# Performance work log

Hardware: AMD Instinct MI355X
Metric: run time of the kernel (lower is better)

Reference implementation:

```python
import jax, jax.numpy as jnp
import numpy as np

N_NODES = 50000
N_EDGES = 1600000
N_GRAPHS = 128
EDGE_DIM = 43
IN_DIM = 35
H = 128          # hidden_dim_1 = hidden_dim_2 = hidden_dim_3
G1, G2 = 64, 32  # gate MLP dims
H6, H7, H8 = 256, 128, 64
U0, U1 = 64, 64  # u_shape


def _linear_params(key, out_dim, in_dim):
    k1, k2 = jax.random.split(key)
    bound = 1.0 / np.sqrt(in_dim)
    W = jax.random.uniform(k1, (out_dim, in_dim), minval=-bound, maxval=bound, dtype=jnp.float32)
    b = jax.random.uniform(k2, (out_dim,), minval=-bound, maxval=bound, dtype=jnp.float32)
    return W, b


def setup_inputs() -> dict:
    key = jax.random.key(0)
    ks = jax.random.split(key, 24)
    x = jax.random.normal(ks[0], (N_NODES, IN_DIM), dtype=jnp.float32)
    edge_index = jax.random.randint(ks[1], (2, N_EDGES), 0, N_NODES, dtype=jnp.int64)
    edge_attr = jax.random.normal(ks[2], (N_EDGES, EDGE_DIM), dtype=jnp.float32)
    batch = jnp.sort(jax.random.randint(ks[3], (N_NODES,), 0, N_GRAPHS, dtype=jnp.int64))
    batch = batch.at[0].set(0).at[-1].set(N_GRAPHS - 1)
    u_soap = jax.random.normal(ks[4], (N_GRAPHS, U0), dtype=jnp.float32)
    u_dimer = jax.random.normal(ks[5], (N_GRAPHS, U1), dtype=jnp.float32)

    W1n, b1n = _linear_params(ks[6], H, IN_DIM + EDGE_DIM)
    W1r, b1r = _linear_params(ks[7], H, IN_DIM)
    W2n, b2n = _linear_params(ks[8], H, H + EDGE_DIM)
    W2r, b2r = _linear_params(ks[9], H, H)
    W3n, b3n = _linear_params(ks[10], H, H + EDGE_DIM)
    W3r, b3r = _linear_params(ks[11], H, H)
    Wg1, bg1 = _linear_params(ks[12], G1, H)
    Wg2, bg2 = _linear_params(ks[13], G2, G1)
    Wg3, bg3 = _linear_params(ks[14], 1, G2)
    Wl1, bl1 = _linear_params(ks[15], H6, U0 + U1 + H)
    Wl2, bl2 = _linear_params(ks[16], H7, H6)
    Wl3, bl3 = _linear_params(ks[17], H8, H7)
    Wl, bl = _linear_params(ks[18], 4, H8)

    return dict(x=x, edge_attr=edge_attr, u_soap=u_soap, u_dimer=u_dimer,
                W1n=W1n, b1n=b1n, W1r=W1r, b1r=b1r,
                W2n=W2n, b2n=b2n, W2r=W2r, b2r=b2r,
                W3n=W3n, b3n=b3n, W3r=W3r, b3r=b3r,
                Wg1=Wg1, bg1=bg1, Wg2=Wg2, bg2=bg2, Wg3=Wg3, bg3=bg3,
                Wl1=Wl1, bl1=bl1, Wl2=Wl2, bl2=bl2, Wl3=Wl3, bl3=bl3,
                Wl=Wl, bl=bl,
                edge_index=edge_index, batch=batch)


def _conv(x, src, edge_attr, Wn, bn, Wr, br):
    # gather source nodes, concat edge features, linear + tanh, scatter-add back to SOURCE (as in original)
    x_adj = jnp.tanh(jnp.concatenate([x[src], edge_attr], axis=1) @ Wn.T + bn)  # [E, H]
    neg_sum = jax.ops.segment_sum(x_adj, src, num_segments=N_NODES)             # [N, H]
    return jnp.tanh(x @ Wr.T + br) + neg_sum


def _segment_softmax(gate, batch, num_segments):
    m = jax.ops.segment_max(gate[:, 0], batch, num_segments=num_segments)
    g = jnp.exp(gate[:, 0] - m[batch])
    s = jax.ops.segment_sum(g, batch, num_segments=num_segments)
    return (g / (s[batch] + 1e-16))[:, None]


def reference(x, edge_attr, u_soap, u_dimer,
              W1n, b1n, W1r, b1r, W2n, b2n, W2r, b2r, W3n, b3n, W3r, b3r,
              Wg1, bg1, Wg2, bg2, Wg3, bg3,
              Wl1, bl1, Wl2, bl2, Wl3, bl3, Wl, bl,
              edge_index, batch):
    src = edge_index[0]
    h = _conv(x, src, edge_attr, W1n, b1n, W1r, b1r)
    h = _conv(h, src, edge_attr, W2n, b2n, W2r, b2r)
    h = _conv(h, src, edge_attr, W3n, b3n, W3r, b3r)

    # GlobalAttention readout
    g = jax.nn.relu(h @ Wg1.T + bg1)
    g = jax.nn.relu(g @ Wg2.T + bg2)
    gate = g @ Wg3.T + bg3                             # [N, 1]
    att = _segment_softmax(gate, batch, N_GRAPHS)      # [N, 1]
    embedding = jax.ops.segment_sum(att * h, batch, num_segments=N_GRAPHS)  # [G, H]

    u = jnp.concatenate([u_soap[:, :U0], u_dimer[:, :U1]], axis=1)
    e2 = jnp.concatenate([embedding, u], axis=1)
    out = jax.nn.relu(e2 @ Wl1.T + bl1)
    out = jax.nn.relu(out @ Wl2.T + bl2)
    out = jax.nn.relu(out @ Wl3.T + bl3)
    out4 = out @ Wl.T + bl                             # [G, 4]
    pred_last = out4.sum(axis=1, keepdims=True)
    return jnp.concatenate([out4, pred_last], axis=1), att
```

## Files before the change

kernel.cpp:

```cpp
#include <hip/hip_runtime.h>
#include <cstdint>
#include <cstddef>

#define N_NODES_C 50000
#define N_EDGES_C 1600000
#define N_GRAPHS_C 128
#define EDGE_DIM_C 43
#define IN_DIM_C 35
#define HDIM_C 128
#define MAXG_C 150000

typedef _Float16 f16x8 __attribute__((ext_vector_type(8)));
typedef float f32x4 __attribute__((ext_vector_type(4)));

__device__ __forceinline__ float fast_tanh(float x) {
    float xc = fminf(9.0f, fmaxf(-9.0f, x));
    float t = __expf(2.0f * xc);
    return (t - 1.0f) * __builtin_amdgcn_rcpf(t + 1.0f);
}


__global__ __launch_bounds__(256) void hist_kernel(const int* __restrict__ src,
                                                   int* __restrict__ cnt) {
    int i = blockIdx.x * 256 + threadIdx.x;
    if (i < N_EDGES_C) atomicAdd(&cnt[src[i]], 1);
}

__global__ __launch_bounds__(1024) void scan_kernel(const int* __restrict__ cnt,
                                                    int* __restrict__ rowptr,
                                                    int* __restrict__ work,
                                                    int* __restrict__ growptr,
                                                    int* __restrict__ ngroups) {
    __shared__ int wsumA[16], wsumB[16];
    __shared__ int carryA, carryB;
    int t = threadIdx.x;
    int lane = t & 63, wid = t >> 6;
    if (t == 0) { carryA = 0; carryB = 0; }
    __syncthreads();
    for (int base = 0; base < N_NODES_C; base += 4096) {
        int i0 = base + t * 4;
        int v[4], u[4];
        #pragma unroll
        for (int j = 0; j < 4; ++j) {
            int i = i0 + j;
            v[j] = (i < N_NODES_C) ? cnt[i] : 0;
            u[j] = (v[j] + 15) >> 4;
        }
        int pv[4], pu[4];
        pv[0] = 0; pu[0] = 0;
        #pragma unroll
        for (int j = 1; j < 4; ++j) { pv[j] = pv[j-1] + v[j-1]; pu[j] = pu[j-1] + u[j-1]; }
        int tA = pv[3] + v[3], tB = pu[3] + u[3];
        int x = tA, y = tB;
        #pragma unroll
        for (int off = 1; off < 64; off <<= 1) {
            int xx = __shfl_up(x, off, 64);
            int yy = __shfl_up(y, off, 64);
            if (lane >= off) { x += xx; y += yy; }
        }
        if (lane == 63) { wsumA[wid] = x; wsumB[wid] = y; }
        __syncthreads();
        if (wid == 0) {
            int wa = (lane < 16) ? wsumA[lane] : 0;
            int wb = (lane < 16) ? wsumB[lane] : 0;
            #pragma unroll
            for (int off = 1; off < 16; off <<= 1) {
                int aa = __shfl_up(wa, off, 64);
                int bb = __shfl_up(wb, off, 64);
                if (lane >= off) { wa += aa; wb += bb; }
            }
            if (lane < 16) { wsumA[lane] = wa; wsumB[lane] = wb; }
        }
        __syncthreads();
        int exA = carryA + (wid ? wsumA[wid - 1] : 0) + x - tA;
        int exB = carryB + (wid ? wsumB[wid - 1] : 0) + y - tB;
        #pragma unroll
        for (int j = 0; j < 4; ++j) {
            int i = i0 + j;
            if (i < N_NODES_C) {
                int rv = exA + pv[j];
                rowptr[i] = rv; work[i] = rv;
                growptr[i] = exB + pu[j];
            }
        }
        int totA = wsumA[15], totB = wsumB[15];
        __syncthreads();
        if (t == 0) { carryA += totA; carryB += totB; }
        __syncthreads();
    }
    if (t == 0) {
        rowptr[N_NODES_C] = carryA;
        growptr[N_NODES_C] = carryB;
        ngroups[0] = carryB;
    }
}

__global__ __launch_bounds__(256) void scatter_kernel(const int* __restrict__ src,
                                                      int* __restrict__ work,
                                                      int* __restrict__ epos) {
    int i = blockIdx.x * 256 + threadIdx.x;
    if (i < N_EDGES_C) {
        int s = src[i];
        int pos = atomicAdd(&work[s], 1);
        epos[i] = pos;
    }
}

__global__ __launch_bounds__(256) void graph_misc(const int* __restrict__ rowptr,
                                                  const int* __restrict__ growptr,
                                                  const int* __restrict__ batch,
                                                  int2* __restrict__ nmeta,
                                                  int* __restrict__ grp) {
    int i = blockIdx.x * 256 + threadIdx.x;
    if (i < N_NODES_C) {
        int deg = rowptr[i + 1] - rowptr[i];
        nmeta[i] = make_int2(deg, growptr[i]);
    }
    if (i <= N_GRAPHS_C) {
        int lo = 0, hi = N_NODES_C;
        while (lo < hi) {
            int mid = (lo + hi) >> 1;
            if (batch[mid] < i) lo = mid + 1; else hi = mid;
        }
        grp[i] = lo;
    }
}

__global__ __launch_bounds__(256) void pad_zero(const int2* __restrict__ nmeta,
                                                _Float16* __restrict__ EAp) {
    int id = blockIdx.x * 256 + threadIdx.x;
    int n = id >> 4, row = id & 15;
    if (n >= N_NODES_C) return;
    int2 nm = nmeta[n];
    int deg = nm.x;
    if (deg == 0) return;
    int rem = deg & 15;
    if (rem == 0 || row < rem) return;
    int g = nm.y + ((deg + 15) >> 4) - 1;
    uint2* dst = (uint2*)(EAp + (size_t)g * 768 + row * 48);
    uint2 z = make_uint2(0u, 0u);
    #pragma unroll
    for (int j = 0; j < 12; ++j) dst[j] = z;
}

__global__ __launch_bounds__(256) void permute_ea(const float* __restrict__ EA,
                                                  const int* __restrict__ src,
                                                  const int* __restrict__ epos,
                                                  const int* __restrict__ rowptr,
                                                  const int* __restrict__ growptr,
                                                  _Float16* __restrict__ EAp) {
    int t = threadIdx.x;
    int e = blockIdx.x * 64 + (t >> 2);
    int q = t & 3;
    if (e >= N_EDGES_C) return;
    int node = src[e];
    int pos = epos[e];
    int r = pos - rowptr[node];
    int g = growptr[node] + (r >> 4);
    int row = r & 15;

    const float* pe = EA + (size_t)e * EDGE_DIM_C;
    unsigned int pk[6];
    #pragma unroll
    for (int jj = 0; jj < 6; ++jj) {
        int c0 = q * 12 + 2 * jj;
        float v0 = (c0 < EDGE_DIM_C) ? pe[c0] : 0.0f;
        float v1 = (c0 + 1 < EDGE_DIM_C) ? pe[c0 + 1] : 0.0f;
        unsigned short h0 = __builtin_bit_cast(unsigned short, (_Float16)v0);
        unsigned short h1 = __builtin_bit_cast(unsigned short, (_Float16)v1);
        pk[jj] = (unsigned int)h0 | ((unsigned int)h1 << 16);
    }
    unsigned int* outp = (unsigned int*)(EAp + (size_t)g * 768 + row * 48 + q * 12);
    *(uint2*)(outp)     = make_uint2(pk[0], pk[1]);
    *(uint2*)(outp + 2) = make_uint2(pk[2], pk[3]);
    *(uint2*)(outp + 4) = make_uint2(pk[4], pk[5]);
}


#define BKN 32
__global__ __launch_bounds__(256) void node_gemm(
    const float* __restrict__ A, int K,
    const float* __restrict__ Wn, int ldn, const float* __restrict__ bn,
    const float* __restrict__ Wr, const float* __restrict__ br,
    float* __restrict__ Base, float* __restrict__ Root)
{
    __shared__ float At[BKN][64];
    __shared__ float Bw[BKN][128];
    int t = threadIdx.x;
    int z = blockIdx.y;
    const float* W = z ? Wr : Wn;
    int ldW = z ? K : ldn;
    const float* bias = z ? br : bn;
    float* Out = z ? Root : Base;

    int m0 = blockIdx.x * 64;
    int tn4 = (t % 32) * 4;
    int tm8 = (t / 32) * 8;
    float acc[8][4];
    #pragma unroll
    for (int a = 0; a < 8; a++)
        #pragma unroll
        for (int b = 0; b < 4; b++) acc[a][b] = 0.0f;

    int nkc = (K + BKN - 1) / BKN;
    for (int c = 0; c < nkc; c++) {
        int kc = c * BKN;
        {
            int m_l = t >> 2;
            int q = t & 3;
            int m = m0 + m_l;
            #pragma unroll
            for (int ii = 0; ii < 8; ii++) {
                int kk = q * 8 + ii;
                int k = kc + kk;
                float v = 0.0f;
                if (m < N_NODES_C && k < K) v = A[(size_t)m * K + k];
                At[kk][m_l] = v;
            }
        }
        {
            int j = t % 128;
            int kg2 = t / 128;
            #pragma unroll
            for (int ii = 0; ii < 16; ii++) {
                int kk = kg2 * 16 + ii;
                int k = kc + kk;
                float v = 0.0f;
                if (k < K) v = W[(size_t)j * ldW + k];
                Bw[kk][j] = v;
            }
        }
        __syncthreads();
        #pragma unroll
        for (int kk = 0; kk < BKN; kk++) {
            float a[8], b[4];
            #pragma unroll
            for (int mi = 0; mi < 8; mi++) a[mi] = At[kk][tm8 + mi];
            #pragma unroll
            for (int ni = 0; ni < 4; ni++) b[ni] = Bw[kk][tn4 + ni];
            #pragma unroll
            for (int mi = 0; mi < 8; mi++)
                #pragma unroll
                for (int ni = 0; ni < 4; ni++)
                    acc[mi][ni] = fmaf(a[mi], b[ni], acc[mi][ni]);
        }
        __syncthreads();
    }

    float4 bv = *(const float4*)&bias[tn4];
    #pragma unroll
    for (int mi = 0; mi < 8; mi++) {
        int m = m0 + tm8 + mi;
        if (m < N_NODES_C) {
            float4 o;
            o.x = acc[mi][0] + bv.x;
            o.y = acc[mi][1] + bv.y;
            o.z = acc[mi][2] + bv.z;
            o.w = acc[mi][3] + bv.w;
            if (z) { o.x = fast_tanh(o.x); o.y = fast_tanh(o.y); o.z = fast_tanh(o.z); o.w = fast_tanh(o.w); }
            *(float4*)&Out[(size_t)m * HDIM_C + tn4] = o;
        }
    }
}


__global__ __launch_bounds__(256) void edge_mfma(
    const _Float16* __restrict__ EAp, const int2* __restrict__ nmeta,
    const float* __restrict__ Base, const float* __restrict__ Root,
    const float* __restrict__ Wfull, int colOff, int ldW,
    float* __restrict__ Hout)
{
    int t = threadIdx.x;
    int lane = t & 63, wid = t >> 6;
    int l15 = lane & 15, quad = lane >> 4;

    f16x8 bf[8][2];
    #pragma unroll
    for (int nt = 0; nt < 8; ++nt) {
        const float* wr = Wfull + (size_t)(nt * 16 + l15) * ldW + colOff;
        #pragma unroll
        for (int kt = 0; kt < 2; ++kt) {
            f16x8 b;
            #pragma unroll
            for (int j = 0; j < 8; ++j) {
                int k = kt * 32 + quad * 8 + j;
                float v = (k < EDGE_DIM_C) ? wr[k] : 0.0f;
                b[j] = (_Float16)v;
            }
            bf[nt][kt] = b;
        }
    }

    int aoff0 = l15 * 48 + quad * 8;
    int aoff1 = l15 * 48 + 32 + ((quad & 1) * 8);
    bool useA1 = (quad < 2);

    int nstride = gridDim.x * 4;
    for (int n = blockIdx.x * 4 + wid; n < N_NODES_C; n += nstride) {
        int2 nm = nmeta[n];
        int deg = nm.x, gptr = nm.y;
        const float* bp = Base + (size_t)n * HDIM_C;
        float bv[8];
        #pragma unroll
        for (int nt = 0; nt < 8; ++nt) bv[nt] = bp[nt * 16 + l15];
        float cs[8];
        #pragma unroll
        for (int nt = 0; nt < 8; ++nt) cs[nt] = 0.0f;

        int ngr = (deg + 15) >> 4;
        int rbase = quad * 4;
        if (ngr > 0) {
            const _Float16* apb = EAp + (size_t)gptr * 768;
            f16x8 zz8 = {};
            f16x8 a0 = *(const f16x8*)(apb + aoff0);
            f16x8 a1 = useA1 ? *(const f16x8*)(apb + aoff1) : zz8;
            for (int gi = 0; gi < ngr; ++gi) {
                f16x8 n0 = a0, n1 = a1;
                if (gi + 1 < ngr) {
                    const _Float16* apn = apb + (size_t)(gi + 1) * 768;
                    n0 = *(const f16x8*)(apn + aoff0);
                    n1 = useA1 ? *(const f16x8*)(apn + aoff1) : zz8;
                }
                int valid = deg - gi * 16; if (valid > 16) valid = 16;
                f32x4 acc[8];
                #pragma unroll
                for (int nt = 0; nt < 8; ++nt) {
                    f32x4 zz = {0.f, 0.f, 0.f, 0.f};
                    acc[nt] = __builtin_amdgcn_mfma_f32_16x16x32_f16(a0, bf[nt][0], zz, 0, 0, 0);
                    acc[nt] = __builtin_amdgcn_mfma_f32_16x16x32_f16(a1, bf[nt][1], acc[nt], 0, 0, 0);
                }
                #pragma unroll
                for (int nt = 0; nt < 8; ++nt) {
                    #pragma unroll
                    for (int r = 0; r < 4; ++r) {
                        float v = fast_tanh(acc[nt][r] + bv[nt]);
                        cs[nt] += (rbase + r < valid) ? v : 0.0f;
                    }
                }
                a0 = n0; a1 = n1;
            }
        }
        #pragma unroll
        for (int nt = 0; nt < 8; ++nt) {
            cs[nt] += __shfl_xor(cs[nt], 16, 64);
            cs[nt] += __shfl_xor(cs[nt], 32, 64);
        }
        float v0, v1;
        if (quad == 0)      { v0 = cs[0]; v1 = cs[1]; }
        else if (quad == 1) { v0 = cs[2]; v1 = cs[3]; }
        else if (quad == 2) { v0 = cs[4]; v1 = cs[5]; }
        else                { v0 = cs[6]; v1 = cs[7]; }
        int c0 = quad * 32 + l15;
        size_t rowb = (size_t)n * HDIM_C;
        Hout[rowb + c0]      = Root[rowb + c0] + v0;
        Hout[rowb + c0 + 16] = Root[rowb + c0 + 16] + v1;
    }
}


__global__ __launch_bounds__(256) void gate_kernel(
    const float* __restrict__ h,
    const float* __restrict__ Wg1, const float* __restrict__ bg1,
    const float* __restrict__ Wg2, const float* __restrict__ bg2,
    const float* __restrict__ Wg3, const float* __restrict__ bg3,
    float* __restrict__ gate)
{
    __shared__ float Ht[128][65];
    __shared__ float G1[64][65];
    __shared__ float G2[32][65];
    int t = threadIdx.x;
    int m0 = blockIdx.x * 64;
    #pragma unroll
    for (int ii = 0; ii < 32; ++ii) {
        int flat = ii * 256 + t;
        int k = flat & 127, m = flat >> 7;
        float v = (m0 + m < N_NODES_C) ? h[(size_t)(m0 + m) * HDIM_C + k] : 0.0f;
        Ht[k][m] = v;
    }
    __syncthreads();
    int m = t & 63, slab = t >> 6;
    {
        float a[16];
        #pragma unroll
        for (int jj = 0; jj < 16; ++jj) a[jj] = bg1[slab * 16 + jj];
        for (int k = 0; k < 128; ++k) {
            float hv = Ht[k][m];
            #pragma unroll
            for (int jj = 0; jj < 16; ++jj)
                a[jj] = fmaf(Wg1[(size_t)(slab * 16 + jj) * 128 + k], hv, a[jj]);
        }
        #pragma unroll
        for (int jj = 0; jj < 16; ++jj) G1[slab * 16 + jj][m] = fmaxf(a[jj], 0.0f);
    }
    __syncthreads();
    {
        float b[8];
        #pragma unroll
        for (int jj = 0; jj < 8; ++jj) b[jj] = bg2[slab * 8 + jj];
        for (int k = 0; k < 64; ++k) {
            float gv = G1[k][m];
            #pragma unroll
            for (int jj = 0; jj < 8; ++jj)
                b[jj] = fmaf(Wg2[(size_t)(slab * 8 + jj) * 64 + k], gv, b[jj]);
        }
        #pragma unroll
        for (int jj = 0; jj < 8; ++jj) G2[slab * 8 + jj][m] = fmaxf(b[jj], 0.0f);
    }
    __syncthreads();
    if (t < 64 && m0 + t < N_NODES_C) {
        float s = bg3[0];
        #pragma unroll
        for (int k = 0; k < 32; ++k) s = fmaf(Wg3[k], G2[k][t], s);
        gate[m0 + t] = s;
    }
}


__global__ __launch_bounds__(256) void graph_attn(
    const float* __restrict__ gate, const int* __restrict__ grp,
    const float* __restrict__ h3, float* __restrict__ att_out,
    float* __restrict__ emb)
{
    int g = blockIdx.x;
    int t = threadIdx.x;
    int s = grp[g], e = grp[g + 1];
    __shared__ float red[256];
    __shared__ float attb[256];

    float m = -3.4e38f;
    for (int i = s + t; i < e; i += 256) m = fmaxf(m, gate[i]);
    red[t] = m;
    __syncthreads();
    #pragma unroll
    for (int off = 128; off >= 1; off >>= 1) {
        if (t < off) red[t] = fmaxf(red[t], red[t + off]);
        __syncthreads();
    }
    m = red[0];
    __syncthreads();

    float sum = 0.0f;
    for (int i = s + t; i < e; i += 256) sum += __expf(gate[i] - m);
    red[t] = sum;
    __syncthreads();
    #pragma unroll
    for (int off = 128; off >= 1; off >>= 1) {
        if (t < off) red[t] += red[t + off];
        __syncthreads();
    }
    float scale = 1.0f / (red[0] + 1e-16f);
    __syncthreads();

    int j = t & 127;
    int half = t >> 7;
    float acc = 0.0f;
    for (int base = s; base < e; base += 256) {
        int i = base + t;
        float a = 0.0f;
        if (i < e) {
            a = __expf(gate[i] - m) * scale;
            att_out[i] = a;
        }
        attb[t] = a;
        __syncthreads();
        int cnt = e - base; if (cnt > 256) cnt = 256;
        for (int r = half; r < cnt; r += 2)
            acc = fmaf(attb[r], h3[(size_t)(base + r) * HDIM_C + j], acc);
        __syncthreads();
    }
    red[t] = acc;
    __syncthreads();
    if (t < 128) emb[(size_t)g * 128 + t] = red[t] + red[t + 128];
}


__global__ __launch_bounds__(256) void final_mlp(
    const float* __restrict__ emb, const float* __restrict__ us, const float* __restrict__ ud,
    const float* __restrict__ Wl1, const float* __restrict__ bl1,
    const float* __restrict__ Wl2, const float* __restrict__ bl2,
    const float* __restrict__ Wl3, const float* __restrict__ bl3,
    const float* __restrict__ Wl, const float* __restrict__ bl,
    float* __restrict__ out5)
{
    int g = blockIdx.x;
    int t = threadIdx.x;
    __shared__ float e2[256], o1[256], o2[128], o3[64], o4[4];
    if (t < 128) e2[t] = emb[(size_t)g * 128 + t];
    else if (t < 192) e2[t] = us[(size_t)g * 64 + (t - 128)];
    else e2[t] = ud[(size_t)g * 64 + (t - 192)];
    __syncthreads();
    {
        float s = bl1[t];
        const float* wr = Wl1 + (size_t)t * 256;
        #pragma unroll 8
        for (int k = 0; k < 256; k++) s = fmaf(wr[k], e2[k], s);
        o1[t] = fmaxf(s, 0.0f);
    }
    __syncthreads();
    if (t < 128) {
        float s = bl2[t];
        const float* wr = Wl2 + (size_t)t * 256;
        #pragma unroll 8
        for (int k = 0; k < 256; k++) s = fmaf(wr[k], o1[k], s);
        o2[t] = fmaxf(s, 0.0f);
    }
    __syncthreads();
    if (t < 64) {
        float s = bl3[t];
        const float* wr = Wl3 + (size_t)t * 128;
        #pragma unroll 8
        for (int k = 0; k < 128; k++) s = fmaf(wr[k], o2[k], s);
        o3[t] = fmaxf(s, 0.0f);
    }
    __syncthreads();
    if (t < 4) {
        float s = bl[t];
        const float* wr = Wl + (size_t)t * 64;
        #pragma unroll 8
        for (int k = 0; k < 64; k++) s = fmaf(wr[k], o3[k], s);
        o4[t] = s;
    }
    __syncthreads();
    if (t < 5) {
        float v = (t < 4) ? o4[t] : (o4[0] + o4[1] + o4[2] + o4[3]);
        out5[(size_t)g * 5 + t] = v;
    }
}


extern "C" void kernel_launch(void* const* d_in, const int* in_sizes, int n_in,
                              void* d_out, int out_size, void* d_ws, size_t ws_size,
                              hipStream_t stream) {
    const float* x       = (const float*)d_in[0];
    const float* ea      = (const float*)d_in[1];
    const float* u_soap  = (const float*)d_in[2];
    const float* u_dimer = (const float*)d_in[3];
    const float* W1n = (const float*)d_in[4];   const float* b1n = (const float*)d_in[5];
    const float* W1r = (const float*)d_in[6];   const float* b1r = (const float*)d_in[7];
    const float* W2n = (const float*)d_in[8];   const float* b2n = (const float*)d_in[9];
    const float* W2r = (const float*)d_in[10];  const float* b2r = (const float*)d_in[11];
    const float* W3n = (const float*)d_in[12];  const float* b3n = (const float*)d_in[13];
    const float* W3r = (const float*)d_in[14];  const float* b3r = (const float*)d_in[15];
    const float* Wg1 = (const float*)d_in[16];  const float* bg1 = (const float*)d_in[17];
    const float* Wg2 = (const float*)d_in[18];  const float* bg2 = (const float*)d_in[19];
    const float* Wg3 = (const float*)d_in[20];  const float* bg3 = (const float*)d_in[21];
    const float* Wl1 = (const float*)d_in[22];  const float* bl1 = (const float*)d_in[23];
    const float* Wl2 = (const float*)d_in[24];  const float* bl2 = (const float*)d_in[25];
    const float* Wl3 = (const float*)d_in[26];  const float* bl3 = (const float*)d_in[27];
    const float* Wl  = (const float*)d_in[28];  const float* bl  = (const float*)d_in[29];
    const int* eidx  = (const int*)d_in[30];
    const int* batch = (const int*)d_in[31];
    const int* src = eidx;

    float* out5 = (float*)d_out;
    float* att  = out5 + (size_t)N_GRAPHS_C * 5;

    char* p = (char*)d_ws;
    size_t off = 0;
    auto alloc = [&](size_t bytes) -> void* {
        void* r = p + off;
        off += (bytes + 255) & ~(size_t)255;
        return r;
    };
    int* cnt     = (int*)alloc((size_t)N_NODES_C * 4);
    int* rowptr  = (int*)alloc((size_t)(N_NODES_C + 1) * 4);
    int* growptr = (int*)alloc((size_t)(N_NODES_C + 1) * 4);
    int* work    = (int*)alloc((size_t)N_NODES_C * 4);
    int* epos    = (int*)alloc((size_t)N_EDGES_C * 4);
    int* grp     = (int*)alloc((size_t)(N_GRAPHS_C + 1) * 4);
    int* ngroups = (int*)alloc(256);
    int2* nmeta  = (int2*)alloc((size_t)N_NODES_C * 8);
    float* gate  = (float*)alloc((size_t)N_NODES_C * 4);
    float* emb   = (float*)alloc((size_t)N_GRAPHS_C * 128 * 4);
    float* bufP  = (float*)alloc((size_t)N_NODES_C * HDIM_C * 4);
    float* bufQ  = (float*)alloc((size_t)N_NODES_C * HDIM_C * 4);
    float* bufR  = (float*)alloc((size_t)N_NODES_C * HDIM_C * 4);
    _Float16* EAp = (_Float16*)alloc((size_t)MAXG_C * 768 * 2);

    hipMemsetAsync(cnt, 0, (size_t)N_NODES_C * 4, stream);

    int eblocks = (N_EDGES_C + 255) / 256;
    hist_kernel<<<eblocks, 256, 0, stream>>>(src, cnt);
    scan_kernel<<<1, 1024, 0, stream>>>(cnt, rowptr, work, growptr, ngroups);
    scatter_kernel<<<eblocks, 256, 0, stream>>>(src, work, epos);
    graph_misc<<<(N_NODES_C + 255) / 256, 256, 0, stream>>>(rowptr, growptr, batch, nmeta, grp);
    pad_zero<<<(N_NODES_C * 16 + 255) / 256, 256, 0, stream>>>(nmeta, EAp);
    permute_ea<<<(N_EDGES_C + 63) / 64, 256, 0, stream>>>(ea, src, epos, rowptr, growptr, EAp);

    dim3 ng((N_NODES_C + 63) / 64, 2);
    int egrid = 2048;

    node_gemm<<<ng, 256, 0, stream>>>(x, IN_DIM_C, W1n, IN_DIM_C + EDGE_DIM_C, b1n, W1r, b1r, bufP, bufQ);
    edge_mfma<<<egrid, 256, 0, stream>>>(EAp, nmeta, bufP, bufQ, W1n, IN_DIM_C, IN_DIM_C + EDGE_DIM_C, bufP);
    node_gemm<<<ng, 256, 0, stream>>>(bufP, HDIM_C, W2n, HDIM_C + EDGE_DIM_C, b2n, W2r, b2r, bufQ, bufR);
    edge_mfma<<<egrid, 256, 0, stream>>>(EAp, nmeta, bufQ, bufR, W2n, HDIM_C, HDIM_C + EDGE_DIM_C, bufQ);
    node_gemm<<<ng, 256, 0, stream>>>(bufQ, HDIM_C, W3n, HDIM_C + EDGE_DIM_C, b3n, W3r, b3r, bufP, bufR);
    edge_mfma<<<egrid, 256, 0, stream>>>(EAp, nmeta, bufP, bufR, W3n, HDIM_C, HDIM_C + EDGE_DIM_C, bufP);

    gate_kernel<<<(N_NODES_C + 63) / 64, 256, 0, stream>>>(bufP, Wg1, bg1, Wg2, bg2, Wg3, bg3, gate);
    graph_attn<<<N_GRAPHS_C, 256, 0, stream>>>(gate, grp, bufP, att, emb);
    final_mlp<<<N_GRAPHS_C, 256, 0, stream>>>(emb, u_soap, u_dimer,
                                              Wl1, bl1, Wl2, bl2, Wl3, bl3, Wl, bl, out5);
}
```

Measured before the change: 1.706 ms.

## Replace padded permuted edge-attr layout with index-gathered fp16 edge rows

Stops physically permuting edge attributes into per-node padded 16-row groups. Instead it converts edge attributes to fp16 in original edge order, stores a CSR edge order array from the scatter, and has each edge_mfma wave gather rows through that index. This drops the pad_zero and permute_ea passes and the group-pointer scan. In exchange, each of the three edge_mfma layers now performs scattered 96-byte gathers plus an extra index load per edge instead of contiguous group reads.

```diff
diff --git a/kernel.cpp b/kernel.cpp
--- a/kernel.cpp
+++ b/kernel.cpp
@@ -8,7 +8,6 @@
 #define EDGE_DIM_C 43
 #define IN_DIM_C 35
 #define HDIM_C 128
-#define MAXG_C 150000
 
 typedef _Float16 f16x8 __attribute__((ext_vector_type(8)));
 typedef float f32x4 __attribute__((ext_vector_type(4)));
@@ -28,93 +27,81 @@
 
 __global__ __launch_bounds__(1024) void scan_kernel(const int* __restrict__ cnt,
                                                     int* __restrict__ rowptr,
-                                                    int* __restrict__ work,
-                                                    int* __restrict__ growptr,
-                                                    int* __restrict__ ngroups) {
-    __shared__ int wsumA[16], wsumB[16];
-    __shared__ int carryA, carryB;
+                                                    int* __restrict__ work) {
+    __shared__ int wsum[16];
+    __shared__ int carry;
     int t = threadIdx.x;
     int lane = t & 63, wid = t >> 6;
-    if (t == 0) { carryA = 0; carryB = 0; }
+    if (t == 0) carry = 0;
     __syncthreads();
     for (int base = 0; base < N_NODES_C; base += 4096) {
         int i0 = base + t * 4;
-        int v[4], u[4];
+        int v[4];
         #pragma unroll
         for (int j = 0; j < 4; ++j) {
             int i = i0 + j;
             v[j] = (i < N_NODES_C) ? cnt[i] : 0;
-            u[j] = (v[j] + 15) >> 4;
-        }
-        int pv[4], pu[4];
-        pv[0] = 0; pu[0] = 0;
-        #pragma unroll
-        for (int j = 1; j < 4; ++j) { pv[j] = pv[j-1] + v[j-1]; pu[j] = pu[j-1] + u[j-1]; }
-        int tA = pv[3] + v[3], tB = pu[3] + u[3];
-        int x = tA, y = tB;
+        }
+        int pv[4];
+        pv[0] = 0;
+        #pragma unroll
+        for (int j = 1; j < 4; ++j) pv[j] = pv[j-1] + v[j-1];
+        int tot = pv[3] + v[3];
+        int x = tot;
         #pragma unroll
         for (int off = 1; off < 64; off <<= 1) {
             int xx = __shfl_up(x, off, 64);
-            int yy = __shfl_up(y, off, 64);
-            if (lane >= off) { x += xx; y += yy; }
-        }
-        if (lane == 63) { wsumA[wid] = x; wsumB[wid] = y; }
+            if (lane >= off) x += xx;
+        }
+        if (lane == 63) wsum[wid] = x;
         __syncthreads();
         if (wid == 0) {
-            int wa = (lane < 16) ? wsumA[lane] : 0;
-            int wb = (lane < 16) ? wsumB[lane] : 0;
+            int wa = (lane < 16) ? wsum[lane] : 0;
             #pragma unroll
             for (int off = 1; off < 16; off <<= 1) {
                 int aa = __shfl_up(wa, off, 64);
-                int bb = __shfl_up(wb, off, 64);
-                if (lane >= off) { wa += aa; wb += bb; }
-            }
-            if (lane < 16) { wsumA[lane] = wa; wsumB[lane] = wb; }
-        }
-        __syncthreads();
-        int exA = carryA + (wid ? wsumA[wid - 1] : 0) + x - tA;
-        int exB = carryB + (wid ? wsumB[wid - 1] : 0) + y - tB;
+                if (lane >= off) wa += aa;
+            }
+            if (lane < 16) wsum[lane] = wa;
+        }
+        __syncthreads();
+        int ex = carry + (wid ? wsum[wid - 1] : 0) + x - tot;
         #pragma unroll
         for (int j = 0; j < 4; ++j) {
             int i = i0 + j;
             if (i < N_NODES_C) {
-                int rv = exA + pv[j];
+                int rv = ex + pv[j];
                 rowptr[i] = rv; work[i] = rv;
-                growptr[i] = exB + pu[j];
-            }
-        }
-        int totA = wsumA[15], totB = wsumB[15];
-        __syncthreads();
-        if (t == 0) { carryA += totA; carryB += totB; }
-        __syncthreads();
-    }
-    if (t == 0) {
-        rowptr[N_NODES_C] = carryA;
-        growptr[N_NODES_C] = carryB;
-        ngroups[0] = carryB;
-    }
+            }
+        }
+        int totAll = wsum[15];
+        __syncthreads();
+        if (t == 0) carry += totAll;
+        __syncthreads();
+    }
+    if (t == 0) rowptr[N_NODES_C] = carry;
 }
 
 __global__ __launch_bounds__(256) void scatter_kernel(const int* __restrict__ src,
                                                       int* __restrict__ work,
-                                                      int* __restrict__ epos) {
+                                                      int* __restrict__ eord) {
     int i = blockIdx.x * 256 + threadIdx.x;
     if (i < N_EDGES_C) {
         int s = src[i];
         int pos = atomicAdd(&work[s], 1);
-        epos[i] = pos;
+        eord[pos] = i;
     }
 }
 
 __global__ __launch_bounds__(256) void graph_misc(const int* __restrict__ rowptr,
-                                                  const int* __restrict__ growptr,
                                                   const int* __restrict__ batch,
                                                   int2* __restrict__ nmeta,
                                                   int* __restrict__ grp) {
     int i = blockIdx.x * 256 + threadIdx.x;
     if (i < N_NODES_C) {
-        int deg = rowptr[i + 1] - rowptr[i];
-        nmeta[i] = make_int2(deg, growptr[i]);
+        int rp = rowptr[i];
+        int deg = rowptr[i + 1] - rp;
+        nmeta[i] = make_int2(deg, rp);
     }
     if (i <= N_GRAPHS_C) {
         int lo = 0, hi = N_NODES_C;
@@ -126,39 +113,12 @@
     }
 }
 
-__global__ __launch_bounds__(256) void pad_zero(const int2* __restrict__ nmeta,
-                                                _Float16* __restrict__ EAp) {
-    int id = blockIdx.x * 256 + threadIdx.x;
-    int n = id >> 4, row = id & 15;
-    if (n >= N_NODES_C) return;
-    int2 nm = nmeta[n];
-    int deg = nm.x;
-    if (deg == 0) return;
-    int rem = deg & 15;
-    if (rem == 0 || row < rem) return;
-    int g = nm.y + ((deg + 15) >> 4) - 1;
-    uint2* dst = (uint2*)(EAp + (size_t)g * 768 + row * 48);
-    uint2 z = make_uint2(0u, 0u);
-    #pragma unroll
-    for (int j = 0; j < 12; ++j) dst[j] = z;
-}
-
-__global__ __launch_bounds__(256) void permute_ea(const float* __restrict__ EA,
-                                                  const int* __restrict__ src,
-                                                  const int* __restrict__ epos,
-                                                  const int* __restrict__ rowptr,
-                                                  const int* __restrict__ growptr,
-                                                  _Float16* __restrict__ EAp) {
+__global__ __launch_bounds__(256) void ea2h(const float* __restrict__ EA,
+                                            _Float16* __restrict__ EAh) {
     int t = threadIdx.x;
     int e = blockIdx.x * 64 + (t >> 2);
     int q = t & 3;
     if (e >= N_EDGES_C) return;
-    int node = src[e];
-    int pos = epos[e];
-    int r = pos - rowptr[node];
-    int g = growptr[node] + (r >> 4);
-    int row = r & 15;
-
     const float* pe = EA + (size_t)e * EDGE_DIM_C;
     unsigned int pk[6];
     #pragma unroll
@@ -170,7 +130,7 @@
         unsigned short h1 = __builtin_bit_cast(unsigned short, (_Float16)v1);
         pk[jj] = (unsigned int)h0 | ((unsigned int)h1 << 16);
     }
-    unsigned int* outp = (unsigned int*)(EAp + (size_t)g * 768 + row * 48 + q * 12);
+    unsigned int* outp = (unsigned int*)(EAh + (size_t)e * 48 + q * 12);
     *(uint2*)(outp)     = make_uint2(pk[0], pk[1]);
     *(uint2*)(outp + 2) = make_uint2(pk[2], pk[3]);
     *(uint2*)(outp + 4) = make_uint2(pk[4], pk[5]);
@@ -265,7 +225,8 @@
 
 
 __global__ __launch_bounds__(256) void edge_mfma(
-    const _Float16* __restrict__ EAp, const int2* __restrict__ nmeta,
+    const _Float16* __restrict__ EAh, const int* __restrict__ eord,
+    const int2* __restrict__ nmeta,
     const float* __restrict__ Base, const float* __restrict__ Root,
     const float* __restrict__ Wfull, int colOff, int ldW,
     float* __restrict__ Hout)
@@ -291,14 +252,14 @@
         }
     }
 
-    int aoff0 = l15 * 48 + quad * 8;
-    int aoff1 = l15 * 48 + 32 + ((quad & 1) * 8);
     bool useA1 = (quad < 2);
+    int off0 = quad * 8;
+    int off1 = 32 + ((quad & 1) * 8);
 
     int nstride = gridDim.x * 4;
     for (int n = blockIdx.x * 4 + wid; n < N_NODES_C; n += nstride) {
         int2 nm = nmeta[n];
-        int deg = nm.x, gptr = nm.y;
+        int deg = nm.x, rp = nm.y;
         const float* bp = Base + (size_t)n * HDIM_C;
         float bv[8];
         #pragma unroll
@@ -310,16 +271,22 @@
         int ngr = (deg + 15) >> 4;
         int rbase = quad * 4;
         if (ngr > 0) {
-            const _Float16* apb = EAp + (size_t)gptr * 768;
             f16x8 zz8 = {};
-            f16x8 a0 = *(const f16x8*)(apb + aoff0);
-            f16x8 a1 = useA1 ? *(const f16x8*)(apb + aoff1) : zz8;
+            f16x8 a0 = zz8, a1 = zz8;
+            if (l15 < deg) {
+                int e0 = eord[rp + l15];
+                const _Float16* ap = EAh + (size_t)e0 * 48;
+                a0 = *(const f16x8*)(ap + off0);
+                if (useA1) a1 = *(const f16x8*)(ap + off1);
+            }
             for (int gi = 0; gi < ngr; ++gi) {
-                f16x8 n0 = a0, n1 = a1;
-                if (gi + 1 < ngr) {
-                    const _Float16* apn = apb + (size_t)(gi + 1) * 768;
-                    n0 = *(const f16x8*)(apn + aoff0);
-                    n1 = useA1 ? *(const f16x8*)(apn + aoff1) : zz8;
+                f16x8 n0 = zz8, n1 = zz8;
+                int rn = (gi + 1) * 16 + l15;
+                if (rn < deg) {
+                    int en = eord[rp + rn];
+                    const _Float16* ap = EAh + (size_t)en * 48;
+                    n0 = *(const f16x8*)(ap + off0);
+                    if (useA1) n1 = *(const f16x8*)(ap + off1);
                 }
                 int valid = deg - gi * 16; if (valid > 16) valid = 16;
                 f32x4 acc[8];
@@ -564,38 +531,35 @@
     };
     int* cnt     = (int*)alloc((size_t)N_NODES_C * 4);
     int* rowptr  = (int*)alloc((size_t)(N_NODES_C + 1) * 4);
-    int* growptr = (int*)alloc((size_t)(N_NODES_C + 1) * 4);
     int* work    = (int*)alloc((size_t)N_NODES_C * 4);
-    int* epos    = (int*)alloc((size_t)N_EDGES_C * 4);
+    int* eord    = (int*)alloc((size_t)(N_EDGES_C + 64) * 4);
     int* grp     = (int*)alloc((size_t)(N_GRAPHS_C + 1) * 4);
-    int* ngroups = (int*)alloc(256);
     int2* nmeta  = (int2*)alloc((size_t)N_NODES_C * 8);
     float* gate  = (float*)alloc((size_t)N_NODES_C * 4);
     float* emb   = (float*)alloc((size_t)N_GRAPHS_C * 128 * 4);
     float* bufP  = (float*)alloc((size_t)N_NODES_C * HDIM_C * 4);
     float* bufQ  = (float*)alloc((size_t)N_NODES_C * HDIM_C * 4);
     float* bufR  = (float*)alloc((size_t)N_NODES_C * HDIM_C * 4);
-    _Float16* EAp = (_Float16*)alloc((size_t)MAXG_C * 768 * 2);
+    _Float16* EAh = (_Float16*)alloc((size_t)N_EDGES_C * 48 * 2);
 
     hipMemsetAsync(cnt, 0, (size_t)N_NODES_C * 4, stream);
 
     int eblocks = (N_EDGES_C + 255) / 256;
+    ea2h<<<(N_EDGES_C + 63) / 64, 256, 0, stream>>>(ea, EAh);
     hist_kernel<<<eblocks, 256, 0, stream>>>(src, cnt);
-    scan_kernel<<<1, 1024, 0, stream>>>(cnt, rowptr, work, growptr, ngroups);
-    scatter_kernel<<<eblocks, 256, 0, stream>>>(src, work, epos);
-    graph_misc<<<(N_NODES_C + 255) / 256, 256, 0, stream>>>(rowptr, growptr, batch, nmeta, grp);
-    pad_zero<<<(N_NODES_C * 16 + 255) / 256, 256, 0, stream>>>(nmeta, EAp);
-    permute_ea<<<(N_EDGES_C + 63) / 64, 256, 0, stream>>>(ea, src, epos, rowptr, growptr, EAp);
+    scan_kernel<<<1, 1024, 0, stream>>>(cnt, rowptr, work);
+    scatter_kernel<<<eblocks, 256, 0, stream>>>(src, work, eord);
+    graph_misc<<<(N_NODES_C + 255) / 256, 256, 0, stream>>>(rowptr, batch, nmeta, grp);
 
     dim3 ng((N_NODES_C + 63) / 64, 2);
     int egrid = 2048;
 
     node_gemm<<<ng, 256, 0, stream>>>(x, IN_DIM_C, W1n, IN_DIM_C + EDGE_DIM_C, b1n, W1r, b1r, bufP, bufQ);
-    edge_mfma<<<egrid, 256, 0, stream>>>(EAp, nmeta, bufP, bufQ, W1n, IN_DIM_C, IN_DIM_C + EDGE_DIM_C, bufP);
+    edge_mfma<<<egrid, 256, 0, stream>>>(EAh, eord, nmeta, bufP, bufQ, W1n, IN_DIM_C, IN_DIM_C + EDGE_DIM_C, bufP);
     node_gemm<<<ng, 256, 0, stream>>>(bufP, HDIM_C, W2n, HDIM_C + EDGE_DIM_C, b2n, W2r, b2r, bufQ, bufR);
-    edge_mfma<<<egrid, 256, 0, stream>>>(EAp, nmeta, bufQ, bufR, W2n, HDIM_C, HDIM_C + EDGE_DIM_C, bufQ);
+    edge_mfma<<<egrid, 256, 0, stream>>>(EAh, eord, nmeta, bufQ, bufR, W2n, HDIM_C, HDIM_C + EDGE_DIM_C, bufQ);
     node_gemm<<<ng, 256, 0, stream>>>(bufQ, HDIM_C, W3n, HDIM_C + EDGE_DIM_C, b3n, W3r, b3r, bufP, bufR);
-    edge_mfma<<<egrid, 256, 0, stream>>>(EAp, nmeta, bufP, bufR, W3n, HDIM_C, HDIM_C + EDGE_DIM_C, bufP);
+    edge_mfma<<<egrid, 256, 0, stream>>>(EAh, eord, nmeta, bufP, bufR, W3n, HDIM_C, HDIM_C + EDGE_DIM_C, bufP);
 
     gate_kernel<<<(N_NODES_C + 63) / 64, 256, 0, stream>>>(bufP, Wg1, bg1, Wg2, bg2, Wg3, bg3, gate);
     graph_attn<<<N_GRAPHS_C, 256, 0, stream>>>(gate, grp, bufP, att, emb);
```

New measurement: 1.733 ms. No clear change (+1.6%).
